# Kernel tuning notes

Measured on AMD Instinct MI355X. Metric: run time of the kernel, lower is better.

The kernel has to match this reference:

```python
import jax, jax.numpy as jnp
import numpy as np

NUM_HEADS = 12
D_MODEL = 768
D_HEAD = D_MODEL // NUM_HEADS


def setup_inputs() -> dict:
    key = jax.random.key(0)
    k_x, k_wqkv, k_bqkv, k_wo, k_bo = jax.random.split(key, 5)
    B, S = 1, 4096
    x = jax.random.normal(k_x, (B, S, D_MODEL), dtype=jnp.float32)
    # flax Dense default init: lecun_normal for kernel, zeros for bias
    w_qkv = jax.random.normal(k_wqkv, (D_MODEL, 3 * D_MODEL), dtype=jnp.float32) / np.sqrt(D_MODEL)
    b_qkv = jnp.zeros((3 * D_MODEL,), dtype=jnp.float32)
    w_o = jax.random.normal(k_wo, (D_MODEL, D_MODEL), dtype=jnp.float32) / np.sqrt(D_MODEL)
    b_o = jnp.zeros((D_MODEL,), dtype=jnp.float32)
    return {"x": x, "w_qkv": w_qkv, "b_qkv": b_qkv, "w_o": w_o, "b_o": b_o}


def reference(x, w_qkv, b_qkv, w_o, b_o):
    B, S, _ = x.shape
    H, Dh = NUM_HEADS, D_HEAD
    qkv = jnp.einsum('bsd,de->bse', x, w_qkv) + b_qkv  # [B,S,3*D]
    q, k, v = jnp.split(qkv, 3, axis=-1)
    # [B,S,D] -> [B,H,S,Dh]
    q = q.reshape(B, S, H, Dh).transpose(0, 2, 1, 3)
    k = k.reshape(B, S, H, Dh).transpose(0, 2, 1, 3)
    v = v.reshape(B, S, H, Dh).transpose(0, 2, 1, 3)
    logits = jnp.einsum('bhqd,bhkd->bhqk', q, k) / jnp.sqrt(jnp.float32(Dh))
    weights = jax.nn.softmax(logits, axis=-1)  # deterministic=True -> no dropout
    attn = jnp.einsum('bhqk,bhkd->bhqd', weights, v)
    attn = attn.transpose(0, 2, 1, 3).reshape(B, S, H * Dh)
    return jnp.einsum('bsd,de->bse', attn, w_o) + b_o
```

## Files before the change

### kernel.cpp

```cpp
#include <hip/hip_runtime.h>

typedef unsigned short u16;
typedef __attribute__((ext_vector_type(8))) short bf16x8;
typedef __attribute__((ext_vector_type(4))) float f32x4;

#define CST 0.18033688011112042f

__device__ inline u16 f2bf(float f) {
    unsigned u;
    __builtin_memcpy(&u, &f, 4);
    unsigned r = (u + 0x7FFF + ((u >> 16) & 1)) >> 16;
    return (u16)r;
}
__device__ inline unsigned pack2(float lo, float hi) {
    return (unsigned)f2bf(lo) | ((unsigned)f2bf(hi) << 16);
}
__device__ inline unsigned fbits(float f) {
    unsigned u;
    __builtin_memcpy(&u, &f, 4);
    return u;
}
__device__ inline f32x4 fzero() {
    f32x4 z = {0.f, 0.f, 0.f, 0.f};
    return z;
}
__device__ inline f32x4 mfma16(bf16x8 a, bf16x8 b, f32x4 c) {
    return __builtin_amdgcn_mfma_f32_16x16x32_bf16(a, b, c, 0, 0, 0);
}

__device__ inline void gld_lds16(const u16* g, u16* l) {
    __builtin_amdgcn_global_load_lds(
        reinterpret_cast<const __attribute__((address_space(1))) unsigned int*>(
            reinterpret_cast<uintptr_t>(g)),
        reinterpret_cast<__attribute__((address_space(3))) unsigned int*>(
            static_cast<unsigned int>(reinterpret_cast<uintptr_t>(l))),
        16, 0, 0);
}

#define NB_WQKV (72 * 24)
#define NB_WO   (24 * 24)
#define NB_CVT  (4096 * 768 / 2048)

__global__ __launch_bounds__(256) void prep(const float* __restrict__ x,
                                            const float* __restrict__ w_qkv,
                                            const float* __restrict__ w_o,
                                            u16* __restrict__ xb,
                                            u16* __restrict__ wqkvT,
                                            u16* __restrict__ woT) {
    __shared__ float tile[32][33];
    int bid = blockIdx.x;
    int t = threadIdx.x;
    if (bid < NB_WQKV + NB_WO) {
        const float* in;
        u16* out;
        int bx, by, R, C;
        if (bid < NB_WQKV) {
            in = w_qkv; out = wqkvT; R = 768; C = 2304;
            bx = bid % 72; by = bid / 72;
        } else {
            int b2 = bid - NB_WQKV;
            in = w_o; out = woT; R = 768; C = 768;
            bx = b2 % 24; by = b2 / 24;
        }
        int c0 = bx * 32, r0 = by * 32;
        int tx = t & 31, ty = t >> 5;
#pragma unroll
        for (int j = 0; j < 32; j += 8)
            tile[ty + j][tx] = in[(size_t)(r0 + ty + j) * C + c0 + tx];
        __syncthreads();
#pragma unroll
        for (int j = 0; j < 32; j += 8)
            out[(size_t)(c0 + ty + j) * R + r0 + tx] = f2bf(tile[tx][ty + j]);
    } else {
        int i = (bid - NB_WQKV - NB_WO) * 2048 + t * 8;
        float4 a = *(const float4*)(x + i);
        float4 b = *(const float4*)(x + i + 4);
        uint4 w;
        w.x = pack2(a.x, a.y);
        w.y = pack2(a.z, a.w);
        w.z = pack2(b.x, b.y);
        w.w = pack2(b.z, b.w);
        *(uint4*)(xb + i) = w;
    }
}

__global__ __launch_bounds__(256) void vtrans(const u16* __restrict__ qkv,
                                              u16* __restrict__ vt) {
    __shared__ u16 T[64 * 136];
    int t = threadIdx.x;
    int h = blockIdx.y, kv0 = blockIdx.x * 128;
    {
        int key = t >> 1, ch = (t & 1) * 32;
        const u16* vp = qkv + (size_t)(kv0 + key) * 2304 + 1536 + h * 64 + ch;
        u16 tmp[32];
        *(uint4*)&tmp[0]  = *(const uint4*)vp;
        *(uint4*)&tmp[8]  = *(const uint4*)(vp + 8);
        *(uint4*)&tmp[16] = *(const uint4*)(vp + 16);
        *(uint4*)&tmp[24] = *(const uint4*)(vp + 24);
        int k5 = key & 31, grp = key >> 5;
        int kp = (grp << 5) | (((k5 >> 2) & 3) << 3) | ((k5 >> 4) << 2) | (k5 & 3);
#pragma unroll
        for (int j = 0; j < 32; j++) T[(ch + j) * 136 + kp] = tmp[j];
    }
    __syncthreads();
    {
        int dh = t >> 2, kc = (t & 3) * 32;
        uint4 o0 = *(const uint4*)&T[dh * 136 + kc];
        uint4 o1 = *(const uint4*)&T[dh * 136 + kc + 8];
        uint4 o2 = *(const uint4*)&T[dh * 136 + kc + 16];
        uint4 o3 = *(const uint4*)&T[dh * 136 + kc + 24];
        u16* op = vt + ((size_t)(h * 64 + dh)) * 4096 + kv0 + kc;
        *(uint4*)op = o0;
        *(uint4*)(op + 8) = o1;
        *(uint4*)(op + 16) = o2;
        *(uint4*)(op + 24) = o3;
    }
}

template <int MT, bool OUT_F32, bool SCALE_Q>
__global__ __launch_bounds__(256) void gemm_bt(const u16* __restrict__ A,
                                               const u16* __restrict__ Bt,
                                               const float* __restrict__ bias,
                                               void* __restrict__ Cv,
                                               int M, int N, int K) {
    constexpr int MI = MT / 32;
    constexpr int NA = MT / 64;
    __shared__ u16 As[MT * 32];
    __shared__ u16 Bs[128 * 32];

    int t = threadIdx.x;
    int wave = t >> 6, lane = t & 63, quad = lane >> 4, l16 = lane & 15;
    int mbase = blockIdx.y * MT, nbase = blockIdx.x * 128;
    int mw = (wave & 1) * (MT / 2), nw = (wave >> 1) * 64;

    f32x4 acc[MI][4];
#pragma unroll
    for (int i = 0; i < MI; i++)
#pragma unroll
        for (int j = 0; j < 4; j++) acc[i][j] = fzero();

    int xqs = (lane & 3) ^ ((lane >> 3) & 3);
    const u16* AgL[NA];
    u16* AsL[NA];
#pragma unroll
    for (int j = 0; j < NA; j++) {
        int rl = wave * (MT / 4) + j * 16 + (lane >> 2);
        AgL[j] = A + (size_t)(mbase + rl) * K + xqs * 8;
        AsL[j] = As + wave * (MT / 4) * 32 + j * 512;
    }
    const u16* BgL[2];
    u16* BsL[2];
#pragma unroll
    for (int j = 0; j < 2; j++) {
        int rl = wave * 32 + j * 16 + (lane >> 2);
        BgL[j] = Bt + (size_t)(nbase + rl) * K + xqs * 8;
        BsL[j] = Bs + wave * 1024 + j * 512;
    }

    int xq = quad ^ ((l16 >> 1) & 3);
    int afo[MI], bfo[4];
#pragma unroll
    for (int i = 0; i < MI; i++) afo[i] = (mw + i * 16 + l16) * 32 + xq * 8;
#pragma unroll
    for (int i = 0; i < 4; i++) bfo[i] = (nw + i * 16 + l16) * 32 + xq * 8;

    for (int kt = 0; kt < K; kt += 32) {
#pragma unroll
        for (int j = 0; j < NA; j++) gld_lds16(AgL[j] + kt, AsL[j]);
#pragma unroll
        for (int j = 0; j < 2; j++) gld_lds16(BgL[j] + kt, BsL[j]);
        __syncthreads();

        bf16x8 af[MI], bfr[4];
#pragma unroll
        for (int i = 0; i < MI; i++) af[i] = *(const bf16x8*)&As[afo[i]];
#pragma unroll
        for (int i = 0; i < 4; i++) bfr[i] = *(const bf16x8*)&Bs[bfo[i]];
#pragma unroll
        for (int mi = 0; mi < MI; mi++)
#pragma unroll
            for (int ni = 0; ni < 4; ni++)
                acc[mi][ni] = mfma16(af[mi], bfr[ni], acc[mi][ni]);
        __syncthreads();
    }

#pragma unroll
    for (int ni = 0; ni < 4; ni++) {
        int col = nbase + nw + ni * 16 + l16;
        float bv = bias[col];
        float scale = (SCALE_Q && col < 768) ? CST : 1.0f;
#pragma unroll
        for (int mi = 0; mi < MI; mi++) {
#pragma unroll
            for (int r = 0; r < 4; r++) {
                int row = mbase + mw + mi * 16 + quad * 4 + r;
                float v = (acc[mi][ni][r] + bv) * scale;
                if (OUT_F32)
                    ((float*)Cv)[(size_t)row * N + col] = v;
                else
                    ((u16*)Cv)[(size_t)row * N + col] = f2bf(v);
            }
        }
    }
}

#define SEQ 4096
#define QKV_LD 2304
#define LK 72
#define LV 136

__global__ __launch_bounds__(256, 3) void attn_flash(const u16* __restrict__ qkv,
                                                     const u16* __restrict__ vt,
                                                     u16* __restrict__ attn) {
    __shared__ __align__(16) char smem[35840];
    u16* Ks  = (u16*)smem;
    u16* VTs = (u16*)(smem + 18432);
    __shared__ float Lm[4][64];

    int t = threadIdx.x;
    int wave = t >> 6, lane = t & 63, quad = lane >> 4, l16 = lane & 15;
    int h = blockIdx.y;
    int q0 = blockIdx.x * 64;
    const int QOFF = h * 64, KOFF = 768 + h * 64;

    bf16x8 qf[4][2];
#pragma unroll
    for (int qs = 0; qs < 4; qs++) {
        const u16* qp = qkv + (size_t)(q0 + qs * 16 + l16) * QKV_LD + QOFF + quad * 8;
        qf[qs][0] = *(const bf16x8*)(qp);
        qf[qs][1] = *(const bf16x8*)(qp + 32);
    }

    f32x4 o[4][4];
    float l4[4];
#pragma unroll
    for (int qs = 0; qs < 4; qs++) {
        l4[qs] = 0.f;
#pragma unroll
        for (int j = 0; j < 4; j++) o[qs][j] = fzero();
    }

    int krow = t >> 1, kch = (t & 1) * 32;
    int vdh = t >> 2, vkc = (t & 3) * 32;
    const u16* kg = qkv + (size_t)krow * QKV_LD + KOFF + kch;
    const u16* vg = vt + ((size_t)(h * 64 + vdh)) * SEQ + vkc;
    u16* kd = &Ks[krow * LK + kch];
    u16* vd = &VTs[vdh * LV + vkc];

    for (int kv0 = 0; kv0 < SEQ; kv0 += 128) {
        {
            const u16* kp = kg + (size_t)kv0 * QKV_LD;
            uint4 k0 = *(const uint4*)kp;
            uint4 k1 = *(const uint4*)(kp + 8);
            uint4 k2 = *(const uint4*)(kp + 16);
            uint4 k3 = *(const uint4*)(kp + 24);
            *(uint4*)kd = k0;
            *(uint4*)(kd + 8) = k1;
            *(uint4*)(kd + 16) = k2;
            *(uint4*)(kd + 24) = k3;
            const u16* vp = vg + kv0;
            uint4 v0 = *(const uint4*)vp;
            uint4 v1 = *(const uint4*)(vp + 8);
            uint4 v2 = *(const uint4*)(vp + 16);
            uint4 v3 = *(const uint4*)(vp + 24);
            *(uint4*)vd = v0;
            *(uint4*)(vd + 8) = v1;
            *(uint4*)(vd + 16) = v2;
            *(uint4*)(vd + 24) = v3;
        }
        __syncthreads();

        bf16x8 kf[2][2];
#pragma unroll
        for (int st = 0; st < 2; st++) {
            const u16* kb = &Ks[(wave * 32 + st * 16 + l16) * LK + quad * 8];
            kf[st][0] = *(const bf16x8*)(kb);
            kf[st][1] = *(const bf16x8*)(kb + 32);
        }
        bf16x8 vf[4];
#pragma unroll
        for (int nt = 0; nt < 4; nt++)
            vf[nt] = *(const bf16x8*)&VTs[(nt * 16 + l16) * LV + wave * 32 + quad * 8];

#pragma unroll
        for (int qs = 0; qs < 4; qs++) {
            f32x4 s0 = mfma16(kf[0][0], qf[qs][0], fzero());
            s0 = mfma16(kf[0][1], qf[qs][1], s0);
            f32x4 s1 = mfma16(kf[1][0], qf[qs][0], fzero());
            s1 = mfma16(kf[1][1], qf[qs][1], s1);
            float p00 = exp2f(s0[0]), p01 = exp2f(s0[1]);
            float p02 = exp2f(s0[2]), p03 = exp2f(s0[3]);
            float p10 = exp2f(s1[0]), p11 = exp2f(s1[1]);
            float p12 = exp2f(s1[2]), p13 = exp2f(s1[3]);
            l4[qs] += ((p00 + p01) + (p02 + p03)) + ((p10 + p11) + (p12 + p13));
            uint4 pk;
            pk.x = __builtin_amdgcn_perm(fbits(p01), fbits(p00), 0x07060302u);
            pk.y = __builtin_amdgcn_perm(fbits(p03), fbits(p02), 0x07060302u);
            pk.z = __builtin_amdgcn_perm(fbits(p11), fbits(p10), 0x07060302u);
            pk.w = __builtin_amdgcn_perm(fbits(p13), fbits(p12), 0x07060302u);
            bf16x8 pf;
            __builtin_memcpy(&pf, &pk, 16);
#pragma unroll
            for (int nt = 0; nt < 4; nt++)
                o[qs][nt] = mfma16(pf, vf[nt], o[qs][nt]);
        }
        __syncthreads();
    }

#pragma unroll
    for (int qs = 0; qs < 4; qs++) {
        l4[qs] += __shfl_xor(l4[qs], 16);
        l4[qs] += __shfl_xor(l4[qs], 32);
    }
    if (lane < 16) {
#pragma unroll
        for (int qs = 0; qs < 4; qs++) Lm[wave][qs * 16 + l16] = l4[qs];
    }

    float* M0 = (float*)smem;
    float* M1 = (float*)(smem + 17408);
    __syncthreads();
    if (wave >= 2) {
        float* M = (wave == 2) ? M0 : M1;
#pragma unroll
        for (int qs = 0; qs < 4; qs++)
#pragma unroll
            for (int nt = 0; nt < 4; nt++)
#pragma unroll
                for (int r = 0; r < 4; r++)
                    M[(qs * 16 + quad * 4 + r) * 68 + nt * 16 + l16] = o[qs][nt][r];
    }
    __syncthreads();
    if (wave < 2) {
        float* M = (wave == 0) ? M0 : M1;
#pragma unroll
        for (int qs = 0; qs < 4; qs++)
#pragma unroll
            for (int nt = 0; nt < 4; nt++)
#pragma unroll
                for (int r = 0; r < 4; r++)
                    o[qs][nt][r] += M[(qs * 16 + quad * 4 + r) * 68 + nt * 16 + l16];
    }
    __syncthreads();
    if (wave == 1) {
#pragma unroll
        for (int qs = 0; qs < 4; qs++)
#pragma unroll
            for (int nt = 0; nt < 4; nt++)
#pragma unroll
                for (int r = 0; r < 4; r++)
                    M0[(qs * 16 + quad * 4 + r) * 68 + nt * 16 + l16] = o[qs][nt][r];
    }
    __syncthreads();
    if (wave == 0) {
#pragma unroll
        for (int qs = 0; qs < 4; qs++) {
#pragma unroll
            for (int r = 0; r < 4; r++) {
                int rw = qs * 16 + quad * 4 + r;
                float l = Lm[0][rw] + Lm[1][rw] + Lm[2][rw] + Lm[3][rw];
                float inv = 1.0f / l;
                u16* op = attn + (size_t)(q0 + rw) * 768 + h * 64;
#pragma unroll
                for (int nt = 0; nt < 4; nt++) {
                    float v = o[qs][nt][r] + M0[rw * 68 + nt * 16 + l16];
                    op[nt * 16 + l16] = f2bf(v * inv);
                }
            }
        }
    }
}

extern "C" void kernel_launch(void* const* d_in, const int* in_sizes, int n_in,
                              void* d_out, int out_size, void* d_ws, size_t ws_size,
                              hipStream_t stream) {
    const float* x      = (const float*)d_in[0];
    const float* w_qkv  = (const float*)d_in[1];
    const float* b_qkv  = (const float*)d_in[2];
    const float* w_o    = (const float*)d_in[3];
    const float* b_o    = (const float*)d_in[4];
    float* out = (float*)d_out;

    u16* wqkvT = (u16*)d_ws;
    u16* woT   = wqkvT + (size_t)2304 * 768;
    u16* qkv   = woT + (size_t)768 * 768;
    u16* attnb = qkv + (size_t)4096 * 2304;
    u16* Vt    = attnb + (size_t)4096 * 768;
    u16* xb    = attnb;

    prep<<<dim3(NB_WQKV + NB_WO + NB_CVT), 256, 0, stream>>>(
        x, w_qkv, w_o, xb, wqkvT, woT);

    gemm_bt<128, false, true><<<dim3(2304 / 128, 4096 / 128), 256, 0, stream>>>(
        xb, wqkvT, b_qkv, qkv, 4096, 2304, 768);

    vtrans<<<dim3(SEQ / 128, 12), 256, 0, stream>>>(qkv, Vt);

    attn_flash<<<dim3(SEQ / 64, 12), 256, 0, stream>>>(qkv, Vt, attnb);

    gemm_bt<64, true, false><<<dim3(768 / 128, 4096 / 64), 256, 0, stream>>>(
        attnb, woT, b_o, out, 4096, 768, 768);
}
```

Before: 218.4 us.

## Load K and V fragments directly from global memory, dropping LDS staging

Removes the shared-memory staging of K and V tiles and the two barriers per iteration. Each wave now reads its own MFMA fragments straight from global memory, which works because each wave uses a disjoint 32-key slice. This gets rid of LDS traffic and synchronisation, but the fragment loads are narrower and more scattered, global latency is no longer hidden behind a barrier-coordinated copy, and it relies on L2 to serve the reuse across blocks.

New measurement: 220.0 us. No clear change (+0.7%).

```diff
diff --git a/kernel.cpp b/kernel.cpp
--- a/kernel.cpp
+++ b/kernel.cpp
@@ -206,15 +206,11 @@
 
 #define SEQ 4096
 #define QKV_LD 2304
-#define LK 72
-#define LV 136
 
 __global__ __launch_bounds__(256, 3) void attn_flash(const u16* __restrict__ qkv,
                                                      const u16* __restrict__ vt,
                                                      u16* __restrict__ attn) {
-    __shared__ __align__(16) char smem[35840];
-    u16* Ks  = (u16*)smem;
-    u16* VTs = (u16*)(smem + 18432);
+    __shared__ __align__(16) char smem[34816];
     __shared__ float Lm[4][64];
 
     int t = threadIdx.x;
@@ -240,47 +236,21 @@
         for (int j = 0; j < 4; j++) o[qs][j] = fzero();
     }
 
-    int krow = t >> 1, kch = (t & 1) * 32;
-    int vdh = t >> 2, vkc = (t & 3) * 32;
-    const u16* kg = qkv + (size_t)krow * QKV_LD + KOFF + kch;
-    const u16* vg = vt + ((size_t)(h * 64 + vdh)) * SEQ + vkc;
-    u16* kd = &Ks[krow * LK + kch];
-    u16* vd = &VTs[vdh * LV + vkc];
+    const u16* kp = qkv + (size_t)(wave * 32 + l16) * QKV_LD + KOFF + quad * 8;
+    const u16* vp = vt + (size_t)(h * 64 + l16) * SEQ + wave * 32 + quad * 8;
 
     for (int kv0 = 0; kv0 < SEQ; kv0 += 128) {
-        {
-            const u16* kp = kg + (size_t)kv0 * QKV_LD;
-            uint4 k0 = *(const uint4*)kp;
-            uint4 k1 = *(const uint4*)(kp + 8);
-            uint4 k2 = *(const uint4*)(kp + 16);
-            uint4 k3 = *(const uint4*)(kp + 24);
-            *(uint4*)kd = k0;
-            *(uint4*)(kd + 8) = k1;
-            *(uint4*)(kd + 16) = k2;
-            *(uint4*)(kd + 24) = k3;
-            const u16* vp = vg + kv0;
-            uint4 v0 = *(const uint4*)vp;
-            uint4 v1 = *(const uint4*)(vp + 8);
-            uint4 v2 = *(const uint4*)(vp + 16);
-            uint4 v3 = *(const uint4*)(vp + 24);
-            *(uint4*)vd = v0;
-            *(uint4*)(vd + 8) = v1;
-            *(uint4*)(vd + 16) = v2;
-            *(uint4*)(vd + 24) = v3;
-        }
-        __syncthreads();
-
         bf16x8 kf[2][2];
-#pragma unroll
-        for (int st = 0; st < 2; st++) {
-            const u16* kb = &Ks[(wave * 32 + st * 16 + l16) * LK + quad * 8];
-            kf[st][0] = *(const bf16x8*)(kb);
-            kf[st][1] = *(const bf16x8*)(kb + 32);
-        }
+        kf[0][0] = *(const bf16x8*)(kp);
+        kf[0][1] = *(const bf16x8*)(kp + 32);
+        kf[1][0] = *(const bf16x8*)(kp + 16 * QKV_LD);
+        kf[1][1] = *(const bf16x8*)(kp + 16 * QKV_LD + 32);
         bf16x8 vf[4];
 #pragma unroll
         for (int nt = 0; nt < 4; nt++)
-            vf[nt] = *(const bf16x8*)&VTs[(nt * 16 + l16) * LV + wave * 32 + quad * 8];
+            vf[nt] = *(const bf16x8*)(vp + (size_t)nt * 16 * SEQ);
+        kp += (size_t)128 * QKV_LD;
+        vp += 128;
 
 #pragma unroll
         for (int qs = 0; qs < 4; qs++) {
@@ -304,7 +274,6 @@
             for (int nt = 0; nt < 4; nt++)
                 o[qs][nt] = mfma16(pf, vf[nt], o[qs][nt]);
         }
-        __syncthreads();
     }
 
 #pragma unroll
```
